# Kernel optimization log

Measured on AMD Instinct MI355X. Metric: run time of the kernel, lower is better.

Reference implementation:

```python
import jax, jax.numpy as jnp
import numpy as np

NUM_HEADS = 16
HEAD_DIM = 64
BSZ, SEQ, EMBED = 2, 2048, NUM_HEADS * HEAD_DIM
SCALE = HEAD_DIM ** (-0.5)
NEG = -1e9  # large negative for masked positions (finite, fp16-unsafe values avoided)


def setup_inputs() -> dict:
    key = jax.random.key(0)
    kq, kk, kv = jax.random.split(key, 3)
    q = jax.random.normal(kq, (BSZ, SEQ, EMBED), dtype=jnp.float32)
    k = jax.random.normal(kk, (BSZ, SEQ, EMBED), dtype=jnp.float32)
    v = jax.random.normal(kv, (BSZ, SEQ, EMBED), dtype=jnp.float32)
    # additive causal mask: 0 on/below diagonal, NEG above, shape (bsz,1,tgt,src)
    causal = jnp.where(jnp.tril(jnp.ones((SEQ, SEQ), dtype=bool)), 0.0, NEG).astype(jnp.float32)
    causal = jnp.broadcast_to(causal[None, None], (BSZ, 1, SEQ, SEQ))
    return {"query_states": q, "key_states": k, "value_states": v,
            "causal_attention_mask": causal}


def reference(query_states, key_states, value_states, causal_attention_mask):
    bsz, tgt_len, embed_dim = query_states.shape
    # [b, h, s, d]
    def shape_heads(t):
        return t.reshape(bsz, -1, NUM_HEADS, HEAD_DIM).transpose(0, 2, 1, 3)
    q = shape_heads(query_states * SCALE)
    k = shape_heads(key_states)
    v = shape_heads(value_states)
    # scores: [b, h, tgt, src]
    attn_weights = jnp.einsum('bhqd,bhkd->bhqk', q, k)
    attn_weights = attn_weights + causal_attention_mask  # broadcast over heads
    attn_probs = jax.nn.softmax(attn_weights, axis=-1)
    # dropout p=0.0 / eval mode -> identity
    attn_output = jnp.einsum('bhqk,bhkd->bhqd', attn_probs, v)
    attn_output = attn_output.transpose(0, 2, 1, 3).reshape(bsz, tgt_len, embed_dim)
    return attn_output
```

## Files before the change

kernel.cpp:

```cpp
#include <hip/hip_runtime.h>
#include <hip/hip_bf16.h>
#include <stdint.h>

#define BSZ 2
#define SEQ 2048
#define NHEADS 16
#define HDIM 64
#define EMBED (NHEADS * HDIM)
#define NQT 32

#define QSCALE 0.1803368801111244f
#define C2 11.5416914f

typedef unsigned short u16;
typedef unsigned int u32;
typedef __attribute__((ext_vector_type(8))) short bf16x8;
typedef __attribute__((ext_vector_type(16))) float f32x16;

#define TILE_B 8192
#define WSV_OFF (8ull * 1024 * 1024)

__device__ __forceinline__ u32 pkbf(float x, float y) {
  union { __hip_bfloat162 h; u32 u; } c;
  c.h = __float22bfloat162_rn(make_float2(x, y));
  return c.u;
}

__global__ __launch_bounds__(256) void prep_kv(const float* __restrict__ K,
                                               const float* __restrict__ V,
                                               char* __restrict__ ws) {
  __shared__ float tile[64][68];
  if (blockIdx.x < 2048) {
    const int t = blockIdx.x * 256 + threadIdx.x;
    const int c = t & 7;
    const int h = (t >> 3) & 15;
    const size_t bs = (size_t)(t >> 7);
    const int s = (int)(bs & 2047);
    const int b = (int)(bs >> 11);
    const float* p = K + bs * EMBED + h * HDIM + c * 8;
    const float4 a = *reinterpret_cast<const float4*>(p);
    const float4 d = *reinterpret_cast<const float4*>(p + 4);
    uint4 out;
    out.x = pkbf(a.x, a.y); out.y = pkbf(a.z, a.w);
    out.z = pkbf(d.x, d.y); out.w = pkbf(d.z, d.w);
    const int kt = s >> 6, key = s & 63;
    const int kb = key >> 5;
    const int ks = c >> 1, hi = c & 1;
    const int lane = hi * 32 + (key & 31);
    char* dst = ws + ((size_t)(b * 16 + h) * 32 + kt) * TILE_B +
                ((kb * 4 + ks) * 64 + lane) * 16;
    *reinterpret_cast<uint4*>(dst) = out;
  } else {
    const int blk = blockIdx.x - 2048;
    const int kt = blk & 31, bh = blk >> 5;
    const int b = bh >> 4, h = bh & 15;
    const float* src = V + ((size_t)b * SEQ + kt * 64) * EMBED + h * HDIM;
    const int t = threadIdx.x;
    {
      const int row = t >> 2, c0 = (t & 3) * 16;
      const float* p = src + (size_t)row * EMBED + c0;
#pragma unroll
      for (int j = 0; j < 4; ++j)
        *reinterpret_cast<float4*>(&tile[row][c0 + 4 * j]) =
            *reinterpret_cast<const float4*>(p + 4 * j);
    }
    __syncthreads();
    const int d = t & 63;
#pragma unroll
    for (int halfc = 0; halfc < 2; ++halfc) {
      const int kc = (t >> 6) + halfc * 4;
      const int kb = kc >> 2, hi = kc & 1;
      const int ka0 = kc * 8;
      const int base = kb * 32 + (ka0 & 16) + hi * 4;
      uint4 out;
      out.x = pkbf(tile[base + 0][d], tile[base + 1][d]);
      out.y = pkbf(tile[base + 2][d], tile[base + 3][d]);
      out.z = pkbf(tile[base + 8][d], tile[base + 9][d]);
      out.w = pkbf(tile[base + 10][d], tile[base + 11][d]);
      const int lane = hi * 32 + (d & 31);
      const int db = d >> 5;
      const int ks2 = (kc >> 1) & 1;
      char* dst = ws + WSV_OFF + ((size_t)bh * 32 + kt) * TILE_B +
                  ((kb * 4 + ks2 * 2 + db) * 64 + lane) * 16;
      *reinterpret_cast<uint4*>(dst) = out;
    }
  }
}

__device__ __forceinline__ void stream_step_r(const bf16x8* kf, const bf16x8* vf,
                                              const bf16x8 q0, const bf16x8 q1,
                                              const bf16x8 q2, const bf16x8 q3,
                                              f32x16& o0, f32x16& o1, float& lsum,
                                              int l, int lq, int hi, bool diagq) {
  f32x16 s = {};
  __builtin_amdgcn_s_setprio(1);
  s = __builtin_amdgcn_mfma_f32_32x32x16_bf16(kf[0], q0, s, 0, 0, 0);
  s = __builtin_amdgcn_mfma_f32_32x32x16_bf16(kf[1], q1, s, 0, 0, 0);
  s = __builtin_amdgcn_mfma_f32_32x32x16_bf16(kf[2], q2, s, 0, 0, 0);
  s = __builtin_amdgcn_mfma_f32_32x32x16_bf16(kf[3], q3, s, 0, 0, 0);
  __builtin_amdgcn_s_setprio(0);

  if (diagq) {
#pragma unroll
    for (int r = 0; r < 16; ++r) {
      const int crow = (r & 3) + 8 * (r >> 2) + 4 * hi;
      if (crow > lq) s[r] = -1.0e30f;
    }
  }

  float e[16];
#pragma unroll
  for (int r = 0; r < 16; ++r) e[r] = __builtin_amdgcn_exp2f(s[r] - C2);
  lsum += ((e[0] + e[1]) + (e[2] + e[3])) + ((e[4] + e[5]) + (e[6] + e[7])) +
          ((e[8] + e[9]) + (e[10] + e[11])) + ((e[12] + e[13]) + (e[14] + e[15]));
  union { u32 w[4]; bf16x8 v; } pa0, pa1;
#pragma unroll
  for (int i = 0; i < 4; ++i) {
    pa0.w[i] = pkbf(e[2 * i], e[2 * i + 1]);
    pa1.w[i] = pkbf(e[8 + 2 * i], e[8 + 2 * i + 1]);
  }

  __builtin_amdgcn_s_setprio(1);
  o0 = __builtin_amdgcn_mfma_f32_32x32x16_bf16(pa0.v, vf[0], o0, 0, 0, 0);
  o1 = __builtin_amdgcn_mfma_f32_32x32x16_bf16(pa0.v, vf[1], o1, 0, 0, 0);
  o0 = __builtin_amdgcn_mfma_f32_32x32x16_bf16(pa1.v, vf[2], o0, 0, 0, 0);
  o1 = __builtin_amdgcn_mfma_f32_32x32x16_bf16(pa1.v, vf[3], o1, 0, 0, 0);
  __builtin_amdgcn_s_setprio(0);
}

__global__ __launch_bounds__(256, 3) void mha_fwd(const float* __restrict__ Q,
                                                  const char* __restrict__ ws,
                                                  float* __restrict__ O) {
  __shared__ __align__(16) float Obuf[4 * 1024 + 64];

  const int id = ((blockIdx.x & 7) << 7) | (blockIdx.x >> 3);
  const int bh = id >> 5;
  const int qt = 31 - (id & 31);
  const int b = bh >> 4, h = bh & 15;

  const int wv = threadIdx.x >> 6;
  const int l = threadIdx.x & 63;
  const int qhalf = wv & 1, kb = wv >> 1;
  const int lq = l & 31;
  const int hi = l >> 5;

  bf16x8 qf[4];
  {
    union { uint4 u; bf16x8 v; } cv;
    const float* qp =
        Q + ((size_t)b * SEQ + qt * 64 + qhalf * 32 + lq) * EMBED + h * HDIM + hi * 8;
#pragma unroll
    for (int ks = 0; ks < 4; ++ks) {
      const float4 a = *reinterpret_cast<const float4*>(qp + ks * 16);
      const float4 d = *reinterpret_cast<const float4*>(qp + ks * 16 + 4);
      cv.u.x = pkbf(a.x * QSCALE, a.y * QSCALE);
      cv.u.y = pkbf(a.z * QSCALE, a.w * QSCALE);
      cv.u.z = pkbf(d.x * QSCALE, d.y * QSCALE);
      cv.u.w = pkbf(d.z * QSCALE, d.w * QSCALE);
      qf[ks] = cv.v;
    }
  }

  const char* gKw = ws + (size_t)bh * 32 * TILE_B + kb * 4096 + l * 16;
  const char* gVw = ws + WSV_OFF + (size_t)bh * 32 * TILE_B + kb * 4096 + l * 16;

#define LOADF(kf, vf, t_)                                                     \
  {                                                                           \
    const char* pK = gKw + (size_t)(t_) * TILE_B;                             \
    const char* pV = gVw + (size_t)(t_) * TILE_B;                             \
    kf[0] = *reinterpret_cast<const bf16x8*>(pK);                             \
    kf[1] = *reinterpret_cast<const bf16x8*>(pK + 1024);                      \
    kf[2] = *reinterpret_cast<const bf16x8*>(pK + 2048);                      \
    kf[3] = *reinterpret_cast<const bf16x8*>(pK + 3072);                      \
    vf[0] = *reinterpret_cast<const bf16x8*>(pV);                             \
    vf[1] = *reinterpret_cast<const bf16x8*>(pV + 1024);                      \
    vf[2] = *reinterpret_cast<const bf16x8*>(pV + 2048);                      \
    vf[3] = *reinterpret_cast<const bf16x8*>(pV + 3072);                      \
  }

  f32x16 o0 = {}, o1 = {};
  float lsum = 0.f;

#define PROC(kf, vf, t_)                                                      \
  {                                                                           \
    const int t = (t_);                                                       \
    const bool dg = (t == qt);                                                \
    if (!(dg && kb == 1 && qhalf == 0))                                       \
      stream_step_r(kf, vf, qf[0], qf[1], qf[2], qf[3], o0, o1, lsum,         \
                    l, lq, hi, dg && (kb == qhalf));                          \
  }

  bf16x8 kfA[4], vfA[4], kfB[4], vfB[4];
  LOADF(kfA, vfA, 0);
  int kt = 0;
  for (; kt + 1 <= qt; kt += 2) {
    LOADF(kfB, vfB, kt + 1);
    PROC(kfA, vfA, kt);
    if (kt + 2 <= qt) LOADF(kfA, vfA, kt + 2);
    PROC(kfB, vfB, kt + 1);
  }
  if (kt <= qt) PROC(kfA, vfA, kt);

  const float l2 = lsum + __shfl_xor(lsum, 32, 64);
  float* Lbuf = Obuf + 4 * 1024;

  if (kb == 1) {
#pragma unroll
    for (int r = 0; r < 16; ++r) {
      Obuf[(qhalf * 2 + 0) * 1024 + r * 64 + l] = o0[r];
      Obuf[(qhalf * 2 + 1) * 1024 + r * 64 + l] = o1[r];
    }
    if (l < 32) Lbuf[qhalf * 32 + lq] = l2;
  }
  __syncthreads();
  if (kb == 0) {
    const float linv = 1.0f / (l2 + Lbuf[qhalf * 32 + lq]);
    const float* Ob = Obuf + (qhalf * 2) * 1024;
    float* outg = O + ((size_t)b * SEQ + qt * 64 + qhalf * 32) * EMBED + h * HDIM;
#pragma unroll
    for (int r = 0; r < 16; ++r) {
      const int crow = (r & 3) + 8 * (r >> 2) + 4 * hi;
      const float il = __shfl(linv, crow, 64);
      outg[(size_t)crow * EMBED + lq] = (o0[r] + Ob[r * 64 + l]) * il;
      outg[(size_t)crow * EMBED + 32 + lq] = (o1[r] + Ob[1024 + r * 64 + l]) * il;
    }
  }
#undef LOADF
#undef PROC
}

extern "C" void kernel_launch(void* const* d_in, const int* in_sizes, int n_in,
                              void* d_out, int out_size, void* d_ws, size_t ws_size,
                              hipStream_t stream) {
  const float* q = (const float*)d_in[0];
  const float* k = (const float*)d_in[1];
  const float* v = (const float*)d_in[2];
  float* o = (float*)d_out;
  char* ws = (char*)d_ws;

  prep_kv<<<dim3(3072), dim3(256), 0, stream>>>(k, v, ws);
  mha_fwd<<<dim3(1024), dim3(256), 0, stream>>>(q, ws, o);
}
```

Before: 54.02 us.

## Balance causal attention work by pairing mirrored 32-row query tiles per block

Each block now handles two 32-row query sub-tiles, sub-tile 63-j and sub-tile j, so every block gets roughly the same number of KV tiles under the causal mask. The combined KV range is split evenly across the four waves. Each wave processes 64-key steps (8 K/V fragments), and partial outputs and row sums are merged through LDS atomics before normalisation. This removes the triangular load imbalance and the tail effect between blocks. In exchange it adds more register pressure (occupancy hint lowered from 3 to 2), per-phase Q reloads, and shared-memory atomic traffic for the reduction.

```diff
diff --git a/kernel.cpp b/kernel.cpp
--- a/kernel.cpp
+++ b/kernel.cpp
@@ -7,7 +7,6 @@
 #define NHEADS 16
 #define HDIM 64
 #define EMBED (NHEADS * HDIM)
-#define NQT 32
 
 #define QSCALE 0.1803368801111244f
 #define C2 11.5416914f
@@ -87,146 +86,185 @@
   }
 }
 
-__device__ __forceinline__ void stream_step_r(const bf16x8* kf, const bf16x8* vf,
-                                              const bf16x8 q0, const bf16x8 q1,
-                                              const bf16x8 q2, const bf16x8 q3,
-                                              f32x16& o0, f32x16& o1, float& lsum,
-                                              int l, int lq, int hi, bool diagq) {
-  f32x16 s = {};
+__device__ __forceinline__ void step64(const bf16x8* kf, const bf16x8* vf,
+                                       const bf16x8* q,
+                                       f32x16& o0, f32x16& o1, float& lsum,
+                                       int lq, int hi, bool diag, int qpar) {
+  const bool do1 = !(diag && qpar == 0);
+  f32x16 s0 = {}, s1 = {};
   __builtin_amdgcn_s_setprio(1);
-  s = __builtin_amdgcn_mfma_f32_32x32x16_bf16(kf[0], q0, s, 0, 0, 0);
-  s = __builtin_amdgcn_mfma_f32_32x32x16_bf16(kf[1], q1, s, 0, 0, 0);
-  s = __builtin_amdgcn_mfma_f32_32x32x16_bf16(kf[2], q2, s, 0, 0, 0);
-  s = __builtin_amdgcn_mfma_f32_32x32x16_bf16(kf[3], q3, s, 0, 0, 0);
+  s0 = __builtin_amdgcn_mfma_f32_32x32x16_bf16(kf[0], q[0], s0, 0, 0, 0);
+  s0 = __builtin_amdgcn_mfma_f32_32x32x16_bf16(kf[1], q[1], s0, 0, 0, 0);
+  s0 = __builtin_amdgcn_mfma_f32_32x32x16_bf16(kf[2], q[2], s0, 0, 0, 0);
+  s0 = __builtin_amdgcn_mfma_f32_32x32x16_bf16(kf[3], q[3], s0, 0, 0, 0);
+  if (do1) {
+    s1 = __builtin_amdgcn_mfma_f32_32x32x16_bf16(kf[4], q[0], s1, 0, 0, 0);
+    s1 = __builtin_amdgcn_mfma_f32_32x32x16_bf16(kf[5], q[1], s1, 0, 0, 0);
+    s1 = __builtin_amdgcn_mfma_f32_32x32x16_bf16(kf[6], q[2], s1, 0, 0, 0);
+    s1 = __builtin_amdgcn_mfma_f32_32x32x16_bf16(kf[7], q[3], s1, 0, 0, 0);
+  }
   __builtin_amdgcn_s_setprio(0);
 
-  if (diagq) {
+  if (diag) {
 #pragma unroll
     for (int r = 0; r < 16; ++r) {
       const int crow = (r & 3) + 8 * (r >> 2) + 4 * hi;
-      if (crow > lq) s[r] = -1.0e30f;
-    }
-  }
-
-  float e[16];
-#pragma unroll
-  for (int r = 0; r < 16; ++r) e[r] = __builtin_amdgcn_exp2f(s[r] - C2);
-  lsum += ((e[0] + e[1]) + (e[2] + e[3])) + ((e[4] + e[5]) + (e[6] + e[7])) +
-          ((e[8] + e[9]) + (e[10] + e[11])) + ((e[12] + e[13]) + (e[14] + e[15]));
-  union { u32 w[4]; bf16x8 v; } pa0, pa1;
-#pragma unroll
-  for (int i = 0; i < 4; ++i) {
-    pa0.w[i] = pkbf(e[2 * i], e[2 * i + 1]);
-    pa1.w[i] = pkbf(e[8 + 2 * i], e[8 + 2 * i + 1]);
+      if (crow > lq) { if (qpar == 0) s0[r] = -1.0e30f; else s1[r] = -1.0e30f; }
+    }
+  }
+
+  union { u32 w[4]; bf16x8 v; } pa00, pa01, pa10, pa11;
+  {
+    float e[16];
+#pragma unroll
+    for (int r = 0; r < 16; ++r) e[r] = __builtin_amdgcn_exp2f(s0[r] - C2);
+    lsum += ((e[0] + e[1]) + (e[2] + e[3])) + ((e[4] + e[5]) + (e[6] + e[7])) +
+            ((e[8] + e[9]) + (e[10] + e[11])) + ((e[12] + e[13]) + (e[14] + e[15]));
+#pragma unroll
+    for (int i = 0; i < 4; ++i) {
+      pa00.w[i] = pkbf(e[2 * i], e[2 * i + 1]);
+      pa01.w[i] = pkbf(e[8 + 2 * i], e[8 + 2 * i + 1]);
+    }
+  }
+  if (do1) {
+    float e[16];
+#pragma unroll
+    for (int r = 0; r < 16; ++r) e[r] = __builtin_amdgcn_exp2f(s1[r] - C2);
+    lsum += ((e[0] + e[1]) + (e[2] + e[3])) + ((e[4] + e[5]) + (e[6] + e[7])) +
+            ((e[8] + e[9]) + (e[10] + e[11])) + ((e[12] + e[13]) + (e[14] + e[15]));
+#pragma unroll
+    for (int i = 0; i < 4; ++i) {
+      pa10.w[i] = pkbf(e[2 * i], e[2 * i + 1]);
+      pa11.w[i] = pkbf(e[8 + 2 * i], e[8 + 2 * i + 1]);
+    }
   }
 
   __builtin_amdgcn_s_setprio(1);
-  o0 = __builtin_amdgcn_mfma_f32_32x32x16_bf16(pa0.v, vf[0], o0, 0, 0, 0);
-  o1 = __builtin_amdgcn_mfma_f32_32x32x16_bf16(pa0.v, vf[1], o1, 0, 0, 0);
-  o0 = __builtin_amdgcn_mfma_f32_32x32x16_bf16(pa1.v, vf[2], o0, 0, 0, 0);
-  o1 = __builtin_amdgcn_mfma_f32_32x32x16_bf16(pa1.v, vf[3], o1, 0, 0, 0);
+  o0 = __builtin_amdgcn_mfma_f32_32x32x16_bf16(pa00.v, vf[0], o0, 0, 0, 0);
+  o1 = __builtin_amdgcn_mfma_f32_32x32x16_bf16(pa00.v, vf[1], o1, 0, 0, 0);
+  o0 = __builtin_amdgcn_mfma_f32_32x32x16_bf16(pa01.v, vf[2], o0, 0, 0, 0);
+  o1 = __builtin_amdgcn_mfma_f32_32x32x16_bf16(pa01.v, vf[3], o1, 0, 0, 0);
+  if (do1) {
+    o0 = __builtin_amdgcn_mfma_f32_32x32x16_bf16(pa10.v, vf[4], o0, 0, 0, 0);
+    o1 = __builtin_amdgcn_mfma_f32_32x32x16_bf16(pa10.v, vf[5], o1, 0, 0, 0);
+    o0 = __builtin_amdgcn_mfma_f32_32x32x16_bf16(pa11.v, vf[6], o0, 0, 0, 0);
+    o1 = __builtin_amdgcn_mfma_f32_32x32x16_bf16(pa11.v, vf[7], o1, 0, 0, 0);
+  }
   __builtin_amdgcn_s_setprio(0);
 }
 
-__global__ __launch_bounds__(256, 3) void mha_fwd(const float* __restrict__ Q,
+__global__ __launch_bounds__(256, 2) void mha_fwd(const float* __restrict__ Q,
                                                   const char* __restrict__ ws,
                                                   float* __restrict__ O) {
-  __shared__ __align__(16) float Obuf[4 * 1024 + 64];
+  __shared__ float M[2][32][64];
+  __shared__ float Ls[2][32];
 
   const int id = ((blockIdx.x & 7) << 7) | (blockIdx.x >> 3);
-  const int bh = id >> 5;
-  const int qt = 31 - (id & 31);
+  const int j = id & 31, bh = id >> 5;
   const int b = bh >> 4, h = bh & 15;
 
-  const int wv = threadIdx.x >> 6;
-  const int l = threadIdx.x & 63;
-  const int qhalf = wv & 1, kb = wv >> 1;
+  const int tid = threadIdx.x;
+  const int wv = tid >> 6;
+  const int l = tid & 63;
   const int lq = l & 31;
   const int hi = l >> 5;
 
-  bf16x8 qf[4];
-  {
-    union { uint4 u; bf16x8 v; } cv;
-    const float* qp =
-        Q + ((size_t)b * SEQ + qt * 64 + qhalf * 32 + lq) * EMBED + h * HDIM + hi * 8;
-#pragma unroll
-    for (int ks = 0; ks < 4; ++ks) {
-      const float4 a = *reinterpret_cast<const float4*>(qp + ks * 16);
-      const float4 d = *reinterpret_cast<const float4*>(qp + ks * 16 + 4);
-      cv.u.x = pkbf(a.x * QSCALE, a.y * QSCALE);
-      cv.u.y = pkbf(a.z * QSCALE, a.w * QSCALE);
-      cv.u.z = pkbf(d.x * QSCALE, d.y * QSCALE);
-      cv.u.w = pkbf(d.z * QSCALE, d.w * QSCALE);
-      qf[ks] = cv.v;
-    }
-  }
-
-  const char* gKw = ws + (size_t)bh * 32 * TILE_B + kb * 4096 + l * 16;
-  const char* gVw = ws + WSV_OFF + (size_t)bh * 32 * TILE_B + kb * 4096 + l * 16;
-
-#define LOADF(kf, vf, t_)                                                     \
+  {
+    float* Mf = &M[0][0][0];
+    for (int i = tid; i < 4096; i += 256) Mf[i] = 0.f;
+    if (tid < 64) (&Ls[0][0])[tid] = 0.f;
+  }
+  __syncthreads();
+
+  const int Th = ((63 - j) >> 1) + 1;
+  const int i0 = (33 * wv + 3) >> 2;
+  const int i1 = (33 * (wv + 1) + 3) >> 2;
+
+  const char* gK = ws + (size_t)bh * 32 * TILE_B;
+  const char* gV = ws + WSV_OFF + (size_t)bh * 32 * TILE_B;
+
+#define LOADK(kf, t_)                                                         \
   {                                                                           \
-    const char* pK = gKw + (size_t)(t_) * TILE_B;                             \
-    const char* pV = gVw + (size_t)(t_) * TILE_B;                             \
-    kf[0] = *reinterpret_cast<const bf16x8*>(pK);                             \
-    kf[1] = *reinterpret_cast<const bf16x8*>(pK + 1024);                      \
-    kf[2] = *reinterpret_cast<const bf16x8*>(pK + 2048);                      \
-    kf[3] = *reinterpret_cast<const bf16x8*>(pK + 3072);                      \
-    vf[0] = *reinterpret_cast<const bf16x8*>(pV);                             \
-    vf[1] = *reinterpret_cast<const bf16x8*>(pV + 1024);                      \
-    vf[2] = *reinterpret_cast<const bf16x8*>(pV + 2048);                      \
-    vf[3] = *reinterpret_cast<const bf16x8*>(pV + 3072);                      \
-  }
-
-  f32x16 o0 = {}, o1 = {};
-  float lsum = 0.f;
-
-#define PROC(kf, vf, t_)                                                      \
+    const char* p_ = gK + (size_t)(t_) * TILE_B + l * 16;                     \
+    _Pragma("unroll") for (int f_ = 0; f_ < 8; ++f_)                          \
+        kf[f_] = *reinterpret_cast<const bf16x8*>(p_ + f_ * 1024);            \
+  }
+#define LOADV(vf, t_)                                                         \
   {                                                                           \
-    const int t = (t_);                                                       \
-    const bool dg = (t == qt);                                                \
-    if (!(dg && kb == 1 && qhalf == 0))                                       \
-      stream_step_r(kf, vf, qf[0], qf[1], qf[2], qf[3], o0, o1, lsum,         \
-                    l, lq, hi, dg && (kb == qhalf));                          \
-  }
-
-  bf16x8 kfA[4], vfA[4], kfB[4], vfB[4];
-  LOADF(kfA, vfA, 0);
-  int kt = 0;
-  for (; kt + 1 <= qt; kt += 2) {
-    LOADF(kfB, vfB, kt + 1);
-    PROC(kfA, vfA, kt);
-    if (kt + 2 <= qt) LOADF(kfA, vfA, kt + 2);
-    PROC(kfB, vfB, kt + 1);
-  }
-  if (kt <= qt) PROC(kfA, vfA, kt);
-
-  const float l2 = lsum + __shfl_xor(lsum, 32, 64);
-  float* Lbuf = Obuf + 4 * 1024;
-
-  if (kb == 1) {
-#pragma unroll
-    for (int r = 0; r < 16; ++r) {
-      Obuf[(qhalf * 2 + 0) * 1024 + r * 64 + l] = o0[r];
-      Obuf[(qhalf * 2 + 1) * 1024 + r * 64 + l] = o1[r];
-    }
-    if (l < 32) Lbuf[qhalf * 32 + lq] = l2;
-  }
-  __syncthreads();
-  if (kb == 0) {
-    const float linv = 1.0f / (l2 + Lbuf[qhalf * 32 + lq]);
-    const float* Ob = Obuf + (qhalf * 2) * 1024;
-    float* outg = O + ((size_t)b * SEQ + qt * 64 + qhalf * 32) * EMBED + h * HDIM;
+    const char* p_ = gV + (size_t)(t_) * TILE_B + l * 16;                     \
+    _Pragma("unroll") for (int f_ = 0; f_ < 8; ++f_)                          \
+        vf[f_] = *reinterpret_cast<const bf16x8*>(p_ + f_ * 1024);            \
+  }
+
+  auto phase = [&](int sub, int kv0, int kv1) {
+    if (kv0 >= kv1) return;
+    const int qpar = sub & 1;
+    const int D = sub >> 1;
+    bf16x8 q[4];
+    {
+      union { uint4 u; bf16x8 v; } cv;
+      const float* qp =
+          Q + ((size_t)b * SEQ + sub * 32 + lq) * EMBED + h * HDIM + hi * 8;
+#pragma unroll
+      for (int ks = 0; ks < 4; ++ks) {
+        const float4 a = *reinterpret_cast<const float4*>(qp + ks * 16);
+        const float4 d = *reinterpret_cast<const float4*>(qp + ks * 16 + 4);
+        cv.u.x = pkbf(a.x * QSCALE, a.y * QSCALE);
+        cv.u.y = pkbf(a.z * QSCALE, a.w * QSCALE);
+        cv.u.z = pkbf(d.x * QSCALE, d.y * QSCALE);
+        cv.u.w = pkbf(d.z * QSCALE, d.w * QSCALE);
+        q[ks] = cv.v;
+      }
+    }
+    f32x16 o0 = {}, o1 = {};
+    float lsum = 0.f;
+    bf16x8 kA[8], kB[8], vv[8];
+    LOADK(kA, kv0);
+    int kv = kv0;
+    for (; kv + 1 < kv1; kv += 2) {
+      LOADK(kB, kv + 1);
+      LOADV(vv, kv);
+      step64(kA, vv, q, o0, o1, lsum, lq, hi, kv == D, qpar);
+      if (kv + 2 < kv1) LOADK(kA, kv + 2);
+      LOADV(vv, kv + 1);
+      step64(kB, vv, q, o0, o1, lsum, lq, hi, kv + 1 == D, qpar);
+    }
+    if (kv < kv1) {
+      LOADV(vv, kv);
+      step64(kA, vv, q, o0, o1, lsum, lq, hi, kv == D, qpar);
+    }
+    const int st = (sub == j) ? 1 : 0;
+    lsum += __shfl_xor(lsum, 32, 64);
 #pragma unroll
     for (int r = 0; r < 16; ++r) {
       const int crow = (r & 3) + 8 * (r >> 2) + 4 * hi;
-      const float il = __shfl(linv, crow, 64);
-      outg[(size_t)crow * EMBED + lq] = (o0[r] + Ob[r * 64 + l]) * il;
-      outg[(size_t)crow * EMBED + 32 + lq] = (o1[r] + Ob[1024 + r * 64 + l]) * il;
-    }
-  }
-#undef LOADF
-#undef PROC
+      atomicAdd(&M[st][crow][lq], o0[r]);
+      atomicAdd(&M[st][crow][32 + lq], o1[r]);
+    }
+    if (hi == 0) atomicAdd(&Ls[st][lq], lsum);
+  };
+
+  {
+    const int a0 = i0, a1 = (i1 < Th) ? i1 : Th;
+    phase(63 - j, a0, a1);
+    const int b0 = (i0 > Th) ? i0 : Th, b1 = i1;
+    phase(j, b0 - Th, b1 - Th);
+  }
+
+  __syncthreads();
+
+  {
+    const int st = tid >> 7;
+    const int q = (tid >> 2) & 31;
+    const int dg = (tid & 3) * 16;
+    const int sub = st ? j : 63 - j;
+    const float linv = 1.0f / Ls[st][q];
+    float* outg = O + ((size_t)b * SEQ + sub * 32 + q) * EMBED + h * HDIM + dg;
+#pragma unroll
+    for (int d = 0; d < 16; ++d) outg[d] = M[st][q][dg + d] * linv;
+  }
+#undef LOADK
+#undef LOADV
 }
 
 extern "C" void kernel_launch(void* const* d_in, const int* in_sizes, int n_in,
```

Result: slower. 94.41 us (+74.8%).
